# Kernel tuning notes

Hardware: AMD Instinct MI355X
Metric: run time of the kernel (lower is better)

The kernel has to match this reference:

```python
import jax, jax.numpy as jnp
import numpy as np
import math

# dims
B, L, D = 2, 2048, 1024          # batch, seq len, embedding_dim
HID, ATT, H = 1024, 512, 8       # linear_hidden_dim, attention_dim, num_heads
DQK, DUV = ATT // H, HID // H    # 64, 128
NBUCK = 64                       # time_num_buckets
MAX_SPAN = 86400 * 90            # max_time_span
EPS = 1e-6
OUT_DIM = 2 * HID + 2 * ATT      # uvqk output dim = 3072


def _time_boundaries():
    # RelativeAttentionBiasModule._build_boundaries: pure log buckets
    steps = NBUCK - 1
    log_part = np.exp(np.linspace(0.0, math.log(MAX_SPAN), steps))
    b = np.unique(np.floor(np.clip(log_part, 1, None)).astype(np.int64)).astype(np.float32)
    return jnp.asarray(b)

_BOUNDARIES = _time_boundaries()  # len <= 63, indices < NBUCK


def setup_inputs() -> dict:
    key = jax.random.key(0)
    ks = jax.random.split(key, 8)
    x = jax.random.normal(ks[0], (B, L, D), dtype=jnp.float32)
    timestamps = jnp.sort(
        jax.random.randint(ks[1], (B, L), 0, 2592000), axis=-1
    )  # chronological event times (seconds)
    attn_mask = jnp.tril(jnp.ones((L, L), dtype=bool))[None].repeat(B, axis=0)  # causal
    W_uvqk = jax.random.normal(ks[2], (OUT_DIM, D), dtype=jnp.float32) * 0.02
    b_uvqk = jnp.zeros((OUT_DIM,), dtype=jnp.float32)
    time_bias = jax.random.normal(ks[3], (NBUCK, H), dtype=jnp.float32) * 0.02
    W_o = jax.random.normal(ks[4], (D, HID), dtype=jnp.float32) * 0.02
    b_o = jnp.zeros((D,), dtype=jnp.float32)
    rms_w = jnp.ones((HID,), dtype=jnp.float32)
    return {"x": x, "timestamps": timestamps, "attn_mask": attn_mask,
            "W_uvqk": W_uvqk, "b_uvqk": b_uvqk, "time_bias": time_bias,
            "W_o": W_o, "b_o": b_o, "rms_w": rms_w}


def reference(x, timestamps, attn_mask, W_uvqk, b_uvqk, time_bias, W_o, b_o, rms_w):
    Bx, Lx, _ = x.shape
    scale = 1.0 / math.sqrt(DQK)

    # fused uvqk projection + act1 (silu)
    h = jax.nn.silu(x @ W_uvqk.T + b_uvqk)  # [B, L, OUT_DIM]
    u, v, q, k = jnp.split(h, [HID, 2 * HID, 2 * HID + ATT], axis=-1)

    def heads(t, d):  # [B, L, H*d] -> [B, H, L, d]
        return t.reshape(Bx, Lx, H, d).transpose(0, 2, 1, 3)

    u = heads(u, DUV)
    v = heads(v, DUV)
    q = heads(q, DQK) * scale
    k = heads(k, DQK)

    logits = jnp.einsum('bhid,bhjd->bhij', q.astype(jnp.float32), k.astype(jnp.float32))

    # bucketized relative-time bias (per-head)
    tdiff = jnp.abs(timestamps[:, :, None] - timestamps[:, None, :])
    tdiff = jnp.clip(tdiff, 1, None).astype(jnp.float32)  # clamp_min(1)
    bk = jnp.searchsorted(_BOUNDARIES, tdiff, side='left')  # torch.bucketize right=False
    rab = time_bias[bk].transpose(0, 3, 1, 2)  # [B, H, L, L]

    # pointwise silu attention (no softmax), masked
    A = jax.nn.silu(logits + rab) * attn_mask[:, None].astype(jnp.float32)

    y = jnp.einsum('bhij,bhjd->bhid', A, v)               # [B, H, L, DUV]
    y = y.transpose(0, 2, 1, 3).reshape(Bx, Lx, HID)       # merge heads
    u_m = u.transpose(0, 2, 1, 3).reshape(Bx, Lx, HID)

    # RMSNorm then U-gate
    rms = y * jax.lax.rsqrt(jnp.mean(y * y, axis=-1, keepdims=True) + EPS) * rms_w
    y_point = rms.astype(x.dtype) * u_m

    return y_point @ W_o.T + b_o  # [B, L, D]
```

## Files before the change

kernel.cpp:

```cpp
#include <hip/hip_runtime.h>
#include <hip/hip_bf16.h>

typedef float f32x4 __attribute__((ext_vector_type(4)));
typedef short s16x8 __attribute__((ext_vector_type(8)));
typedef short s16x4 __attribute__((ext_vector_type(4)));
typedef unsigned short u16x4 __attribute__((ext_vector_type(4)));

__device__ __forceinline__ float bf2f(unsigned short u) {
    union { unsigned int i; float f; } x; x.i = ((unsigned int)u) << 16; return x.f;
}
__device__ __forceinline__ unsigned short f2bf(float f) {
    union { float f; unsigned int i; } x; x.f = f;
    unsigned int r = x.i + 0x7FFFu + ((x.i >> 16) & 1u);
    return (unsigned short)(r >> 16);
}
__device__ __forceinline__ float silu_fast(float v) {
    return v * __builtin_amdgcn_rcpf(1.f + __expf(-v));
}

#define GLDS16(gp, lp) __builtin_amdgcn_global_load_lds( \
    (const __attribute__((address_space(1))) unsigned int*)(gp), \
    (__attribute__((address_space(3))) unsigned int*)(lp), 16, 0, 0)

__global__ __launch_bounds__(256) void cvt_bucketize(
    const float* __restrict__ X, const float* __restrict__ W,
    const float* __restrict__ Wo, const int* __restrict__ TS,
    unsigned short* __restrict__ Xb, unsigned short* __restrict__ Wb,
    unsigned short* __restrict__ Wob, unsigned char* __restrict__ BK)
{
    const int tid = threadIdx.x;
    if (blockIdx.x < 8192) {
        int idx = blockIdx.x * 256 + tid;
        const float* src; unsigned short* dst; int off;
        if (idx < 1048576)       { src = X;  dst = Xb;  off = idx; }
        else if (idx < 1835008)  { src = W;  dst = Wb;  off = idx - 1048576; }
        else                     { src = Wo; dst = Wob; off = idx - 1835008; }
        f32x4 v = *reinterpret_cast<const f32x4*>(&src[(size_t)off * 4]);
        u16x4 o;
        #pragma unroll
        for (int j = 0; j < 4; ++j) o[j] = f2bf(v[j]);
        *reinterpret_cast<u16x4*>(&dst[(size_t)off * 4]) = o;
        return;
    }
    const int bid = blockIdx.x - 8192;
    const int jt = bid & 31, it = (bid >> 5) & 31, b = bid >> 10;
    if (jt > it) return;
    __shared__ int bndRaw[63];
    __shared__ int bnd[64];
    __shared__ int tsi[64], tsj[64];
    if (tid < 63) {
        double step = log(7776000.0) / 62.0;
        double v = exp(step * (double)tid);
        if (v < 1.0) v = 1.0;
        bndRaw[tid] = (int)floor(v);
    }
    if (tid >= 64 && tid < 128) tsi[tid - 64] = TS[b * 2048 + it * 64 + (tid - 64)];
    else if (tid >= 128 && tid < 192) tsj[tid - 128] = TS[b * 2048 + jt * 64 + (tid - 128)];
    __syncthreads();
    if (tid == 0) {
        int c = 0, p = -1;
        for (int i = 0; i < 63; ++i) { int x = bndRaw[i]; if (x != p) { bnd[c++] = x; p = x; } }
        for (; c < 64; ++c) bnd[c] = 0x7FFFFFFF;
    }
    __syncthreads();
    const int il = tid & 63, jc = (tid >> 6) * 16;
    const int tiv = tsi[il];
    unsigned char out[16];
    #pragma unroll
    for (int u = 0; u < 16; ++u) {
        int td = tiv - tsj[jc + u]; td = td < 0 ? -td : td; if (td < 1) td = 1;
        int pos = 0;
        #pragma unroll
        for (int st = 32; st; st >>= 1)
            if (bnd[pos + st - 1] < td) pos += st;
        out[u] = (unsigned char)pos;
    }
    *reinterpret_cast<int4*>(&BK[((size_t)b << 22) + (size_t)(it * 64 + il) * 2048 + jt * 64 + jc]) =
        *reinterpret_cast<const int4*>(out);
}

__global__ __launch_bounds__(512, 2) void gemm_uvqk(
    const unsigned short* __restrict__ Xb, const unsigned short* __restrict__ Wb,
    const float* __restrict__ bias,
    unsigned short* __restrict__ U, unsigned short* __restrict__ Vt,
    unsigned short* __restrict__ Q, unsigned short* __restrict__ K)
{
    __shared__ __align__(16) unsigned short smem[2][2][256][64];
    const int tid = threadIdx.x;
    const int wv = tid >> 6, lane = tid & 63;
    const int g = lane >> 4, lr = lane & 15;
    const int wid = (blockIdx.x & 7) * 24 + (blockIdx.x >> 3);
    const int mt = wid & 15, nt = wid >> 4;
    const int m0 = mt * 256, n0 = nt * 256;
    const int wm = wv >> 2, wn = wv & 3;
    const int ls = lr & 7;
    f32x4 acc[8][4] = {};

    auto stageA = [&](int kt, int db) {
        const int k0 = kt * 64;
        #pragma unroll
        for (int c = 0; c < 4; ++c) {
            int id = c * 512 + tid;
            int row = id >> 3, c8 = id & 7;
            GLDS16(&Xb[(size_t)(m0 + row) * 1024 + k0 + (c8 ^ (row & 7)) * 8],
                   &smem[db][0][row][c8 * 8]);
        }
    };
    auto stageB = [&](int kt, int db) {
        const int k0 = kt * 64;
        #pragma unroll
        for (int c = 0; c < 4; ++c) {
            int id = c * 512 + tid;
            int row = id >> 3, c8 = id & 7;
            GLDS16(&Wb[(size_t)(n0 + row) * 1024 + k0 + (c8 ^ (row & 7)) * 8],
                   &smem[db][1][row][c8 * 8]);
        }
    };

    stageB(0, 0); stageA(0, 0);

    for (int kt = 0; kt < 16; ++kt) {
        const int db = kt & 1;
        const unsigned short (*sA)[64] = smem[db][0];
        const unsigned short (*sB)[64] = smem[db][1];
        s16x8 bfr[4][2];
        #pragma unroll
        for (int q = 0; q < 4; ++q) {
            if (q == 0) {
                if (kt < 15) {
                    stageB(kt + 1, db ^ 1);
                    asm volatile("s_waitcnt vmcnt(4)" ::: "memory");
                } else {
                    asm volatile("s_waitcnt vmcnt(0)" ::: "memory");
                }
                __builtin_amdgcn_s_barrier();
            }
            s16x8 afr[2][2];
            if (q == 0) {
                #pragma unroll
                for (int ni = 0; ni < 4; ++ni)
                    #pragma unroll
                    for (int kq = 0; kq < 2; ++kq)
                        bfr[ni][kq] = *reinterpret_cast<const s16x8*>(
                            &sB[wn * 64 + ni * 16 + lr][((kq * 4 + g) ^ ls) * 8]);
            }
            #pragma unroll
            for (int j = 0; j < 2; ++j)
                #pragma unroll
                for (int kq = 0; kq < 2; ++kq)
                    afr[j][kq] = *reinterpret_cast<const s16x8*>(
                        &sA[wm * 128 + (2 * q + j) * 16 + lr][((kq * 4 + g) ^ ls) * 8]);
            if (q == 1 && kt < 15) stageA(kt + 1, db ^ 1);
            asm volatile("s_waitcnt lgkmcnt(0)" ::: "memory");
            __builtin_amdgcn_sched_barrier(0);
            __builtin_amdgcn_s_setprio(1);
            #pragma unroll
            for (int kq = 0; kq < 2; ++kq)
                #pragma unroll
                for (int j = 0; j < 2; ++j)
                    #pragma unroll
                    for (int ni = 0; ni < 4; ++ni)
                        acc[2 * q + j][ni] = __builtin_amdgcn_mfma_f32_16x16x32_bf16(
                            afr[j][kq], bfr[ni][kq], acc[2 * q + j][ni], 0, 0, 0);
            __builtin_amdgcn_s_setprio(0);
            __builtin_amdgcn_s_barrier();
        }
    }
    __syncthreads();

    if (n0 >= 1024 && n0 < 2048) {
        const int dglob = n0 - 1024 + wn * 64;
        const int head = dglob >> 7, dbase = dglob & 127;
        unsigned short* sT = &smem[0][0][0][0] + wv * 2304;
        #pragma unroll
        for (int mh = 0; mh < 2; ++mh) {
            #pragma unroll
            for (int hh = 0; hh < 2; ++hh) {
                #pragma unroll
                for (int nn = 0; nn < 2; ++nn) {
                    int ni = hh * 2 + nn;
                    float bn = bias[n0 + wn * 64 + ni * 16 + lr];
                    #pragma unroll
                    for (int mi = 0; mi < 4; ++mi)
                        #pragma unroll
                        for (int r = 0; r < 4; ++r)
                            sT[(nn * 16 + lr) * 72 + mi * 16 + g * 4 + r] =
                                f2bf(silu_fast(acc[mh * 4 + mi][ni][r] + bn));
                }
                #pragma unroll
                for (int c = 0; c < 4; ++c) {
                    int id = c * 64 + lane;
                    int row = id >> 3, ch = id & 7;
                    s16x8 val = *reinterpret_cast<const s16x8*>(&sT[row * 72 + ch * 8]);
                    int d = dbase + hh * 32 + row;
                    int mg = m0 + wm * 128 + mh * 64 + ch * 8;
                    int bb = mg >> 11, l = mg & 2047;
                    *reinterpret_cast<s16x8*>(
                        &Vt[(((size_t)(bb * 8 + head) * 128 + d) << 11) + l]) = val;
                }
            }
        }
    } else {
        #pragma unroll
        for (int ni = 0; ni < 4; ++ni) {
            int n = n0 + wn * 64 + ni * 16 + lr;
            float bn = bias[n];
            #pragma unroll
            for (int mi = 0; mi < 8; ++mi) {
                #pragma unroll
                for (int r = 0; r < 4; ++r) {
                    int m = m0 + wm * 128 + mi * 16 + g * 4 + r;
                    float v = silu_fast(acc[mi][ni][r] + bn);
                    int b = m >> 11, l = m & 2047;
                    if (n < 1024) {
                        U[(size_t)m * 1024 + n] = f2bf(v);
                    } else if (n < 2560) {
                        int dd = n - 2048, h = dd >> 6, d = dd & 63;
                        Q[((((size_t)(b * 8 + h) << 11) + l) << 6) + d] = f2bf(v * 0.125f);
                    } else {
                        int dd = n - 2560, h = dd >> 6, d = dd & 63;
                        K[((((size_t)(b * 8 + h) << 11) + l) << 6) + d] = f2bf(v);
                    }
                }
            }
        }
    }
}

__global__ __launch_bounds__(512, 1) void attn(
    const unsigned short* __restrict__ Q, const unsigned short* __restrict__ K,
    const unsigned short* __restrict__ Vt, const unsigned char* __restrict__ BK,
    const float* __restrict__ TB, unsigned short* __restrict__ Y)
{
    __shared__ __align__(16) unsigned short sK[2][2][64][64];
    __shared__ __align__(16) unsigned short sV[2][2][128][64];
    __shared__ __align__(16) unsigned char  sBK[2][2][64][64];

    const int tid = threadIdx.x, wv = tid >> 6, lane = tid & 63;
    const int g = lane >> 4, lr = lane & 15;

    const int bid = blockIdx.x;
    const int xcd = bid & 7, kix = bid >> 3;
    const int bh = 2 * xcd + (kix & 1);
    const int ti = 31 - (kix >> 1);
    const int b = bh >> 3, h = bh & 7;
    const int i0 = ti * 64;
    const int rg = wv & 3;
    const int half = wv >> 2;
    const int irow = i0 + rg * 16;
    const int P = (ti + 2) >> 1;

    const int tbl = __float_as_int(TB[lane * 8 + h]);

    const unsigned short* qb = Q + ((size_t)bh << 11) * 64;
    const unsigned short* kb = K + ((size_t)bh << 11) * 64;
    const unsigned short* vtb = Vt + ((size_t)bh << 7) * 2048;
    const unsigned char* bkb = BK + ((size_t)b << 22);

    s16x8 aq[2];
    #pragma unroll
    for (int kq = 0; kq < 2; ++kq)
        aq[kq] = *reinterpret_cast<const s16x8*>(&qb[(size_t)(irow + lr) * 64 + kq * 32 + g * 8]);

    char* sKb = (char*)&sK[0][0][0][0];
    char* sVb = (char*)&sV[0][0][0][0];
    char* sBKb = (char*)&sBK[0][0][0][0];
    const int cs = lr & 7;
    const int ib = irow + lr;

    auto stage = [&](int q, int db) {
        int jth = 2 * q + half;
        if (jth > ti) jth = 2 * q;
        const size_t j0 = (size_t)jth * 64;
        char* kd = sKb + db * 16384 + half * 8192;
        char* vd = sVb + db * 32768 + half * 16384;
        char* bkd = sBKb + db * 8192 + half * 4096;
        #pragma unroll
        for (int c = 0; c < 2; ++c) {
            int chunk = rg * 128 + c * 64 + lane;
            int row = chunk >> 3, c8 = chunk & 7;
            GLDS16(kb + (j0 + row) * 64 + ((c8 ^ (row & 7)) * 8), kd + chunk * 16);
        }
        #pragma unroll
        for (int c = 0; c < 4; ++c) {
            int chunk = rg * 256 + c * 64 + lane;
            int d = chunk >> 3, c8 = chunk & 7;
            GLDS16(vtb + (size_t)d * 2048 + j0 + ((c8 ^ (d & 7)) * 8), vd + chunk * 16);
        }
        {
            int chunk = rg * 64 + lane;
            int row = chunk >> 2, c16 = chunk & 3;
            GLDS16(bkb + (size_t)(i0 + row) * 2048 + j0 + ((c16 ^ (row & 3)) * 16), bkd + chunk * 16);
        }
    };

    f32x4 accy[8] = {};

#define COMPUTE(DB) { \
        const int jt = 2 * p + half; \
        if (jt <= ti) { \
            const char* kbase = sKb + (DB) * 16384 + half * 8192; \
            f32x4 sacc[4] = {}; \
            _Pragma("unroll") \
            for (int ni = 0; ni < 4; ++ni) { \
                _Pragma("unroll") \
                for (int kq = 0; kq < 2; ++kq) { \
                    s16x8 kf = *reinterpret_cast<const s16x8*>( \
                        kbase + (ni * 16 + lr) * 128 + (((kq * 4 + g) ^ cs) << 4)); \
                    sacc[ni] = __builtin_amdgcn_mfma_f32_16x16x32_bf16(kf, aq[kq], sacc[ni], 0, 0, 0); \
                } \
            } \
            const int j0 = jt * 64; \
            const bool diag = (jt == ti); \
            s16x4 pf[4]; \
            _Pragma("unroll") \
            for (int ni = 0; ni < 4; ++ni) { \
                unsigned int bw = *reinterpret_cast<const unsigned int*>( \
                    sBKb + (DB) * 8192 + half * 4096 + (rg * 16 + lr) * 64 + ((ni ^ (lr & 3)) << 4) + g * 4); \
                float b0 = __int_as_float(__builtin_amdgcn_ds_bpermute((int)((bw & 255u) << 2), tbl)); \
                float b1 = __int_as_float(__builtin_amdgcn_ds_bpermute((int)(((bw >> 8) & 255u) << 2), tbl)); \
                float b2 = __int_as_float(__builtin_amdgcn_ds_bpermute((int)(((bw >> 16) & 255u) << 2), tbl)); \
                float b3 = __int_as_float(__builtin_amdgcn_ds_bpermute((int)((bw >> 24) << 2), tbl)); \
                float v0 = silu_fast(sacc[ni][0] + b0); \
                float v1 = silu_fast(sacc[ni][1] + b1); \
                float v2 = silu_fast(sacc[ni][2] + b2); \
                float v3 = silu_fast(sacc[ni][3] + b3); \
                if (diag) { \
                    int jb = j0 + ni * 16 + g * 4; \
                    if (jb + 0 > ib) v0 = 0.f; \
                    if (jb + 1 > ib) v1 = 0.f; \
                    if (jb + 2 > ib) v2 = 0.f; \
                    if (jb + 3 > ib) v3 = 0.f; \
                } \
                unsigned int w0, w1; \
                asm("v_cvt_pk_bf16_f32 %0, %1, %2" : "=v"(w0) : "v"(v0), "v"(v1)); \
                asm("v_cvt_pk_bf16_f32 %0, %1, %2" : "=v"(w1) : "v"(v2), "v"(v3)); \
                union { unsigned int u_[2]; s16x4 v_; } cvt_; \
                cvt_.u_[0] = w0; cvt_.u_[1] = w1; \
                pf[ni] = cvt_.v_; \
            } \
            const char* vbase = sVb + (DB) * 32768 + half * 16384; \
            _Pragma("unroll") \
            for (int di = 0; di < 8; ++di) { \
                _Pragma("unroll") \
                for (int ni = 0; ni < 4; ++ni) { \
                    s16x4 vf = *reinterpret_cast<const s16x4*>( \
                        vbase + (di * 16 + lr) * 128 + (((2 * ni + (g >> 1)) ^ cs) << 4) + ((g & 1) << 3)); \
                    accy[di] = __builtin_amdgcn_mfma_f32_16x16x16bf16_1k(pf[ni], vf, accy[di], 0, 0, 0); \
                } \
            } \
        } }

    stage(0, 0);

    int p = 0;
    for (;;) {
        __builtin_amdgcn_s_barrier();
        if (p + 1 < P) {
            stage(p + 1, 1);
            asm volatile("s_waitcnt vmcnt(7)" ::: "memory");
        } else {
            asm volatile("s_waitcnt vmcnt(0)" ::: "memory");
        }
        __builtin_amdgcn_s_barrier();
        COMPUTE(0);
        if (++p == P) break;
        __builtin_amdgcn_s_barrier();
        if (p + 1 < P) {
            stage(p + 1, 0);
            asm volatile("s_waitcnt vmcnt(7)" ::: "memory");
        } else {
            asm volatile("s_waitcnt vmcnt(0)" ::: "memory");
        }
        __builtin_amdgcn_s_barrier();
        COMPUTE(1);
        if (++p == P) break;
    }
#undef COMPUTE

    __syncthreads();
    float* red = (float*)sVb;
    if (wv >= 4) {
        #pragma unroll
        for (int di = 0; di < 8; ++di)
            #pragma unroll
            for (int r = 0; r < 4; ++r)
                red[(rg * 16 + g * 4 + r) * 132 + di * 16 + lr] = accy[di][r];
    }
    __syncthreads();
    if (wv < 4) {
        #pragma unroll
        for (int di = 0; di < 8; ++di)
            #pragma unroll
            for (int r = 0; r < 4; ++r) {
                float s = accy[di][r] + red[(rg * 16 + g * 4 + r) * 132 + di * 16 + lr];
                Y[(size_t)((b << 11) + irow + g * 4 + r) * 1024 + h * 128 + di * 16 + lr] = f2bf(s);
            }
    }
}

__global__ __launch_bounds__(256) void rmsnorm_gate(
    const unsigned short* __restrict__ Y, const unsigned short* __restrict__ U,
    const float* __restrict__ rw, unsigned short* __restrict__ YP)
{
    __shared__ float red[4];
    const int row = blockIdx.x, tid = threadIdx.x;
    u16x4 v4 = *reinterpret_cast<const u16x4*>(&Y[(size_t)row * 1024 + tid * 4]);
    float v[4];
    #pragma unroll
    for (int j = 0; j < 4; ++j) v[j] = bf2f(v4[j]);
    float ss = v[0] * v[0] + v[1] * v[1] + v[2] * v[2] + v[3] * v[3];
    #pragma unroll
    for (int off = 32; off; off >>= 1) ss += __shfl_down(ss, off);
    if ((tid & 63) == 0) red[tid >> 6] = ss;
    __syncthreads();
    float rms = rsqrtf((red[0] + red[1] + red[2] + red[3]) * (1.f / 1024.f) + 1e-6f);
    #pragma unroll
    for (int j = 0; j < 4; ++j) {
        int c = tid * 4 + j;
        float o = v[j] * rms * rw[c] * bf2f(U[(size_t)row * 1024 + c]);
        YP[(size_t)row * 1024 + c] = f2bf(o);
    }
}

__global__ __launch_bounds__(512) void gemm_out(
    const unsigned short* __restrict__ YP, const unsigned short* __restrict__ Wob,
    const float* __restrict__ bo, float* __restrict__ OUT)
{
    __shared__ __align__(16) unsigned short sA[128][64];
    __shared__ __align__(16) unsigned short sB[128][64];
    const int tid = threadIdx.x;
    const int wv = tid >> 6, lane = tid & 63;
    const int g = lane >> 4, lr = lane & 15;
    const int wid = (blockIdx.x & 7) * 32 + (blockIdx.x >> 3);
    const int m0 = (wid & 31) * 128, n0 = (wid >> 5) * 128;
    const int wr = (wv >> 2) * 64, wc = (wv & 3) * 32;
    const int ls = lr & 7;
    f32x4 acc[4][2] = {};

    for (int k0 = 0; k0 < 1024; k0 += 64) {
        #pragma unroll
        for (int c = 0; c < 2; ++c) {
            int id = c * 512 + tid;
            int row = id >> 3, c8 = id & 7;
            int sc = (c8 ^ (row & 7)) * 8;
            GLDS16(&YP[(size_t)(m0 + row) * 1024 + k0 + sc], &sA[row][c8 * 8]);
            GLDS16(&Wob[(size_t)(n0 + row) * 1024 + k0 + sc], &sB[row][c8 * 8]);
        }
        __syncthreads();
        #pragma unroll
        for (int kq = 0; kq < 2; ++kq) {
            s16x8 afr[4], bfr[2];
            #pragma unroll
            for (int i = 0; i < 4; ++i)
                afr[i] = *reinterpret_cast<const s16x8*>(
                    &sA[wr + i * 16 + lr][((kq * 4 + g) ^ ls) * 8]);
            #pragma unroll
            for (int i = 0; i < 2; ++i)
                bfr[i] = *reinterpret_cast<const s16x8*>(
                    &sB[wc + i * 16 + lr][((kq * 4 + g) ^ ls) * 8]);
            #pragma unroll
            for (int mi = 0; mi < 4; ++mi)
                #pragma unroll
                for (int ni = 0; ni < 2; ++ni)
                    acc[mi][ni] = __builtin_amdgcn_mfma_f32_16x16x32_bf16(
                        afr[mi], bfr[ni], acc[mi][ni], 0, 0, 0);
        }
        __syncthreads();
    }

    #pragma unroll
    for (int ni = 0; ni < 2; ++ni) {
        int n = n0 + wc + ni * 16 + lr;
        float bn = bo[n];
        #pragma unroll
        for (int mi = 0; mi < 4; ++mi)
            #pragma unroll
            for (int r = 0; r < 4; ++r) {
                int m = m0 + wr + mi * 16 + g * 4 + r;
                OUT[(size_t)m * 1024 + n] = acc[mi][ni][r] + bn;
            }
    }
}

extern "C" void kernel_launch(void* const* d_in, const int* in_sizes, int n_in,
                              void* d_out, int out_size, void* d_ws, size_t ws_size,
                              hipStream_t stream) {
    const float* X     = (const float*)d_in[0];
    const int*   TS    = (const int*)d_in[1];
    const float* Wuvqk = (const float*)d_in[3];
    const float* buvqk = (const float*)d_in[4];
    const float* TB    = (const float*)d_in[5];
    const float* Wo    = (const float*)d_in[6];
    const float* bo    = (const float*)d_in[7];
    const float* rw    = (const float*)d_in[8];
    float* OUT = (float*)d_out;

    char* ws = (char*)d_ws;
    unsigned short* Qb  = (unsigned short*)(ws);
    unsigned short* Kb  = (unsigned short*)(ws + (4u << 20));
    unsigned short* Vt  = (unsigned short*)(ws + (8u << 20));
    unsigned short* Ub  = (unsigned short*)(ws + (16u << 20));
    unsigned short* Yb  = (unsigned short*)(ws + (24u << 20));
    unsigned short* Xb  = (unsigned short*)(ws + (24u << 20));
    unsigned short* Wb  = (unsigned short*)(ws + (32u << 20));
    unsigned short* YP  = (unsigned short*)(ws + (40u << 20));
    unsigned char*  BKm = (unsigned char*)(ws + (48u << 20));
    unsigned short* Wob = (unsigned short*)(ws + (56u << 20));

    cvt_bucketize<<<10240, 256, 0, stream>>>(X, Wuvqk, Wo, TS, Xb, Wb, Wob, BKm);
    gemm_uvqk<<<192, 512, 0, stream>>>(Xb, Wb, buvqk, Ub, Vt, Qb, Kb);
    attn<<<512, 512, 0, stream>>>(Qb, Kb, Vt, BKm, TB, Yb);
    rmsnorm_gate<<<4096, 256, 0, stream>>>(Yb, Ub, rw, YP);
    gemm_out<<<256, 512, 0, stream>>>(YP, Wob, bo, OUT);
}
```

Before: 133.9 us.

## Drop LDS staging in attention; split key tiles across blocks with partial outputs

```diff
diff --git a/kernel.cpp b/kernel.cpp
--- a/kernel.cpp
+++ b/kernel.cpp
@@ -227,188 +227,116 @@
     }
 }
 
-__global__ __launch_bounds__(512, 1) void attn(
+__global__ __launch_bounds__(256, 4) void attn(
     const unsigned short* __restrict__ Q, const unsigned short* __restrict__ K,
     const unsigned short* __restrict__ Vt, const unsigned char* __restrict__ BK,
-    const float* __restrict__ TB, unsigned short* __restrict__ Y)
+    const float* __restrict__ TB,
+    unsigned short* __restrict__ Yb0, unsigned short* __restrict__ Yb1)
 {
-    __shared__ __align__(16) unsigned short sK[2][2][64][64];
-    __shared__ __align__(16) unsigned short sV[2][2][128][64];
-    __shared__ __align__(16) unsigned char  sBK[2][2][64][64];
-
     const int tid = threadIdx.x, wv = tid >> 6, lane = tid & 63;
     const int g = lane >> 4, lr = lane & 15;
 
     const int bid = blockIdx.x;
-    const int xcd = bid & 7, kix = bid >> 3;
-    const int bh = 2 * xcd + (kix & 1);
-    const int ti = 31 - (kix >> 1);
+    const int xcd = bid & 7, u = bid >> 3;
+    const int hp = u & 1, jh = (u >> 1) & 1;
+    const int u2 = u >> 2;
+    const int s = u2 & 7, r_ = u2 >> 3;
+    const int ti = (r_ == 0) ? s : (r_ == 1) ? (15 - s) : (r_ == 2) ? (16 + s) : (31 - s);
+    const int bh = 2 * xcd + hp;
     const int b = bh >> 3, h = bh & 7;
-    const int i0 = ti * 64;
-    const int rg = wv & 3;
-    const int half = wv >> 2;
-    const int irow = i0 + rg * 16;
-    const int P = (ti + 2) >> 1;
+    const int irow = ti * 64 + wv * 16;
 
     const int tbl = __float_as_int(TB[lane * 8 + h]);
 
     const unsigned short* qb = Q + ((size_t)bh << 11) * 64;
     const unsigned short* kb = K + ((size_t)bh << 11) * 64;
     const unsigned short* vtb = Vt + ((size_t)bh << 7) * 2048;
-    const unsigned char* bkb = BK + ((size_t)b << 22);
+    const unsigned char* bkp = BK + ((size_t)b << 22) + (size_t)(irow + lr) * 2048 + g * 4;
+    unsigned short* Yp = jh ? Yb1 : Yb0;
 
     s16x8 aq[2];
     #pragma unroll
     for (int kq = 0; kq < 2; ++kq)
         aq[kq] = *reinterpret_cast<const s16x8*>(&qb[(size_t)(irow + lr) * 64 + kq * 32 + g * 8]);
 
-    char* sKb = (char*)&sK[0][0][0][0];
-    char* sVb = (char*)&sV[0][0][0][0];
-    char* sBKb = (char*)&sBK[0][0][0][0];
-    const int cs = lr & 7;
     const int ib = irow + lr;
-
-    auto stage = [&](int q, int db) {
-        int jth = 2 * q + half;
-        if (jth > ti) jth = 2 * q;
-        const size_t j0 = (size_t)jth * 64;
-        char* kd = sKb + db * 16384 + half * 8192;
-        char* vd = sVb + db * 32768 + half * 16384;
-        char* bkd = sBKb + db * 8192 + half * 4096;
-        #pragma unroll
-        for (int c = 0; c < 2; ++c) {
-            int chunk = rg * 128 + c * 64 + lane;
-            int row = chunk >> 3, c8 = chunk & 7;
-            GLDS16(kb + (j0 + row) * 64 + ((c8 ^ (row & 7)) * 8), kd + chunk * 16);
-        }
-        #pragma unroll
-        for (int c = 0; c < 4; ++c) {
-            int chunk = rg * 256 + c * 64 + lane;
-            int d = chunk >> 3, c8 = chunk & 7;
-            GLDS16(vtb + (size_t)d * 2048 + j0 + ((c8 ^ (d & 7)) * 8), vd + chunk * 16);
-        }
-        {
-            int chunk = rg * 64 + lane;
-            int row = chunk >> 2, c16 = chunk & 3;
-            GLDS16(bkb + (size_t)(i0 + row) * 2048 + j0 + ((c16 ^ (row & 3)) * 16), bkd + chunk * 16);
-        }
-    };
-
     f32x4 accy[8] = {};
 
-#define COMPUTE(DB) { \
-        const int jt = 2 * p + half; \
-        if (jt <= ti) { \
-            const char* kbase = sKb + (DB) * 16384 + half * 8192; \
-            f32x4 sacc[4] = {}; \
-            _Pragma("unroll") \
-            for (int ni = 0; ni < 4; ++ni) { \
-                _Pragma("unroll") \
-                for (int kq = 0; kq < 2; ++kq) { \
-                    s16x8 kf = *reinterpret_cast<const s16x8*>( \
-                        kbase + (ni * 16 + lr) * 128 + (((kq * 4 + g) ^ cs) << 4)); \
-                    sacc[ni] = __builtin_amdgcn_mfma_f32_16x16x32_bf16(kf, aq[kq], sacc[ni], 0, 0, 0); \
-                } \
-            } \
-            const int j0 = jt * 64; \
-            const bool diag = (jt == ti); \
-            s16x4 pf[4]; \
-            _Pragma("unroll") \
-            for (int ni = 0; ni < 4; ++ni) { \
-                unsigned int bw = *reinterpret_cast<const unsigned int*>( \
-                    sBKb + (DB) * 8192 + half * 4096 + (rg * 16 + lr) * 64 + ((ni ^ (lr & 3)) << 4) + g * 4); \
-                float b0 = __int_as_float(__builtin_amdgcn_ds_bpermute((int)((bw & 255u) << 2), tbl)); \
-                float b1 = __int_as_float(__builtin_amdgcn_ds_bpermute((int)(((bw >> 8) & 255u) << 2), tbl)); \
-                float b2 = __int_as_float(__builtin_amdgcn_ds_bpermute((int)(((bw >> 16) & 255u) << 2), tbl)); \
-                float b3 = __int_as_float(__builtin_amdgcn_ds_bpermute((int)((bw >> 24) << 2), tbl)); \
-                float v0 = silu_fast(sacc[ni][0] + b0); \
-                float v1 = silu_fast(sacc[ni][1] + b1); \
-                float v2 = silu_fast(sacc[ni][2] + b2); \
-                float v3 = silu_fast(sacc[ni][3] + b3); \
-                if (diag) { \
-                    int jb = j0 + ni * 16 + g * 4; \
-                    if (jb + 0 > ib) v0 = 0.f; \
-                    if (jb + 1 > ib) v1 = 0.f; \
-                    if (jb + 2 > ib) v2 = 0.f; \
-                    if (jb + 3 > ib) v3 = 0.f; \
-                } \
-                unsigned int w0, w1; \
-                asm("v_cvt_pk_bf16_f32 %0, %1, %2" : "=v"(w0) : "v"(v0), "v"(v1)); \
-                asm("v_cvt_pk_bf16_f32 %0, %1, %2" : "=v"(w1) : "v"(v2), "v"(v3)); \
-                union { unsigned int u_[2]; s16x4 v_; } cvt_; \
-                cvt_.u_[0] = w0; cvt_.u_[1] = w1; \
-                pf[ni] = cvt_.v_; \
-            } \
-            const char* vbase = sVb + (DB) * 32768 + half * 16384; \
-            _Pragma("unroll") \
-            for (int di = 0; di < 8; ++di) { \
-                _Pragma("unroll") \
-                for (int ni = 0; ni < 4; ++ni) { \
-                    s16x4 vf = *reinterpret_cast<const s16x4*>( \
-                        vbase + (di * 16 + lr) * 128 + (((2 * ni + (g >> 1)) ^ cs) << 4) + ((g & 1) << 3)); \
-                    accy[di] = __builtin_amdgcn_mfma_f32_16x16x16bf16_1k(pf[ni], vf, accy[di], 0, 0, 0); \
-                } \
-            } \
-        } }
-
-    stage(0, 0);
-
-    int p = 0;
-    for (;;) {
-        __builtin_amdgcn_s_barrier();
-        if (p + 1 < P) {
-            stage(p + 1, 1);
-            asm volatile("s_waitcnt vmcnt(7)" ::: "memory");
-        } else {
-            asm volatile("s_waitcnt vmcnt(0)" ::: "memory");
-        }
-        __builtin_amdgcn_s_barrier();
-        COMPUTE(0);
-        if (++p == P) break;
-        __builtin_amdgcn_s_barrier();
-        if (p + 1 < P) {
-            stage(p + 1, 0);
-            asm volatile("s_waitcnt vmcnt(7)" ::: "memory");
-        } else {
-            asm volatile("s_waitcnt vmcnt(0)" ::: "memory");
-        }
-        __builtin_amdgcn_s_barrier();
-        COMPUTE(1);
-        if (++p == P) break;
-    }
-#undef COMPUTE
-
-    __syncthreads();
-    float* red = (float*)sVb;
-    if (wv >= 4) {
-        #pragma unroll
-        for (int di = 0; di < 8; ++di)
-            #pragma unroll
-            for (int r = 0; r < 4; ++r)
-                red[(rg * 16 + g * 4 + r) * 132 + di * 16 + lr] = accy[di][r];
-    }
-    __syncthreads();
-    if (wv < 4) {
-        #pragma unroll
-        for (int di = 0; di < 8; ++di)
-            #pragma unroll
-            for (int r = 0; r < 4; ++r) {
-                float s = accy[di][r] + red[(rg * 16 + g * 4 + r) * 132 + di * 16 + lr];
-                Y[(size_t)((b << 11) + irow + g * 4 + r) * 1024 + h * 128 + di * 16 + lr] = f2bf(s);
-            }
-    }
+    for (int jt = jh; jt <= ti; jt += 2) {
+        const int j0 = jt * 64;
+        unsigned int bw[4];
+        #pragma unroll
+        for (int ni = 0; ni < 4; ++ni)
+            bw[ni] = *reinterpret_cast<const unsigned int*>(bkp + j0 + ni * 16);
+        f32x4 sacc[4] = {};
+        #pragma unroll
+        for (int ni = 0; ni < 4; ++ni) {
+            #pragma unroll
+            for (int kq = 0; kq < 2; ++kq) {
+                s16x8 kf = *reinterpret_cast<const s16x8*>(
+                    &kb[(size_t)(j0 + ni * 16 + lr) * 64 + kq * 32 + g * 8]);
+                sacc[ni] = __builtin_amdgcn_mfma_f32_16x16x32_bf16(kf, aq[kq], sacc[ni], 0, 0, 0);
+            }
+        }
+        const bool diag = (jt == ti);
+        s16x4 pf[4];
+        #pragma unroll
+        for (int ni = 0; ni < 4; ++ni) {
+            unsigned int w = bw[ni];
+            float b0 = __int_as_float(__builtin_amdgcn_ds_bpermute((int)((w & 255u) << 2), tbl));
+            float b1 = __int_as_float(__builtin_amdgcn_ds_bpermute((int)(((w >> 8) & 255u) << 2), tbl));
+            float b2 = __int_as_float(__builtin_amdgcn_ds_bpermute((int)(((w >> 16) & 255u) << 2), tbl));
+            float b3 = __int_as_float(__builtin_amdgcn_ds_bpermute((int)((w >> 24) << 2), tbl));
+            float v0 = silu_fast(sacc[ni][0] + b0);
+            float v1 = silu_fast(sacc[ni][1] + b1);
+            float v2 = silu_fast(sacc[ni][2] + b2);
+            float v3 = silu_fast(sacc[ni][3] + b3);
+            if (diag) {
+                int jb = j0 + ni * 16 + g * 4;
+                if (jb + 0 > ib) v0 = 0.f;
+                if (jb + 1 > ib) v1 = 0.f;
+                if (jb + 2 > ib) v2 = 0.f;
+                if (jb + 3 > ib) v3 = 0.f;
+            }
+            unsigned int w0, w1;
+            asm("v_cvt_pk_bf16_f32 %0, %1, %2" : "=v"(w0) : "v"(v0), "v"(v1));
+            asm("v_cvt_pk_bf16_f32 %0, %1, %2" : "=v"(w1) : "v"(v2), "v"(v3));
+            union { unsigned int u_[2]; s16x4 v_; } cvt_;
+            cvt_.u_[0] = w0; cvt_.u_[1] = w1;
+            pf[ni] = cvt_.v_;
+        }
+        #pragma unroll
+        for (int di = 0; di < 8; ++di) {
+            const unsigned short* vrow = vtb + (size_t)(di * 16 + lr) * 2048 + j0 + g * 4;
+            #pragma unroll
+            for (int ni = 0; ni < 4; ++ni) {
+                s16x4 vf = *reinterpret_cast<const s16x4*>(vrow + ni * 16);
+                accy[di] = __builtin_amdgcn_mfma_f32_16x16x16bf16_1k(pf[ni], vf, accy[di], 0, 0, 0);
+            }
+        }
+    }
+
+    #pragma unroll
+    for (int di = 0; di < 8; ++di)
+        #pragma unroll
+        for (int r = 0; r < 4; ++r) {
+            int i = irow + g * 4 + r;
+            Yp[(size_t)((b << 11) + i) * 1024 + h * 128 + di * 16 + lr] = f2bf(accy[di][r]);
+        }
 }
 
 __global__ __launch_bounds__(256) void rmsnorm_gate(
-    const unsigned short* __restrict__ Y, const unsigned short* __restrict__ U,
+    const unsigned short* __restrict__ Y0, const unsigned short* __restrict__ Y1,
+    const unsigned short* __restrict__ U,
     const float* __restrict__ rw, unsigned short* __restrict__ YP)
 {
     __shared__ float red[4];
     const int row = blockIdx.x, tid = threadIdx.x;
-    u16x4 v4 = *reinterpret_cast<const u16x4*>(&Y[(size_t)row * 1024 + tid * 4]);
+    u16x4 a4 = *reinterpret_cast<const u16x4*>(&Y0[(size_t)row * 1024 + tid * 4]);
+    u16x4 b4 = *reinterpret_cast<const u16x4*>(&Y1[(size_t)row * 1024 + tid * 4]);
     float v[4];
     #pragma unroll
-    for (int j = 0; j < 4; ++j) v[j] = bf2f(v4[j]);
+    for (int j = 0; j < 4; ++j) v[j] = bf2f(a4[j]) + bf2f(b4[j]);
     float ss = v[0] * v[0] + v[1] * v[1] + v[2] * v[2] + v[3] * v[3];
     #pragma unroll
     for (int off = 32; off; off >>= 1) ss += __shfl_down(ss, off);
@@ -501,16 +429,17 @@
     unsigned short* Kb  = (unsigned short*)(ws + (4u << 20));
     unsigned short* Vt  = (unsigned short*)(ws + (8u << 20));
     unsigned short* Ub  = (unsigned short*)(ws + (16u << 20));
-    unsigned short* Yb  = (unsigned short*)(ws + (24u << 20));
     unsigned short* Xb  = (unsigned short*)(ws + (24u << 20));
+    unsigned short* Yb0 = (unsigned short*)(ws + (24u << 20));
     unsigned short* Wb  = (unsigned short*)(ws + (32u << 20));
+    unsigned short* Yb1 = (unsigned short*)(ws + (32u << 20));
     unsigned short* YP  = (unsigned short*)(ws + (40u << 20));
     unsigned char*  BKm = (unsigned char*)(ws + (48u << 20));
     unsigned short* Wob = (unsigned short*)(ws + (56u << 20));
 
     cvt_bucketize<<<10240, 256, 0, stream>>>(X, Wuvqk, Wo, TS, Xb, Wb, Wob, BKm);
     gemm_uvqk<<<192, 512, 0, stream>>>(Xb, Wb, buvqk, Ub, Vt, Qb, Kb);
-    attn<<<512, 512, 0, stream>>>(Qb, Kb, Vt, BKm, TB, Yb);
-    rmsnorm_gate<<<4096, 256, 0, stream>>>(Yb, Ub, rw, YP);
+    attn<<<1024, 256, 0, stream>>>(Qb, Kb, Vt, BKm, TB, Yb0, Yb1);
+    rmsnorm_gate<<<4096, 256, 0, stream>>>(Yb0, Yb1, Ub, rw, YP);
     gemm_out<<<256, 512, 0, stream>>>(YP, Wob, bo, OUT);
 }
```

New measurement: 257.4 us. 1.92x slower.
